# Performance work log

Measured on AMD Instinct MI355X. Metric: run time of the kernel, lower is better.

## Reference

```python
import jax, jax.numpy as jnp
import numpy as np

D_MODEL = 2048
NUM_TILES = 64
D_SLICE = D_MODEL // NUM_TILES  # 32
TILES_PER_CLUSTER = 8
NUM_CLUSTERS = NUM_TILES // TILES_PER_CLUSTER  # 8
GRID = 16
LN_EPS = 1e-5

# per-tile owned dimension indices: (tile_id*d_slice + j) % d_model  -> disjoint contiguous slices
DIMS = (np.arange(NUM_TILES)[:, None] * D_SLICE + np.arange(D_SLICE)[None, :]) % D_MODEL  # [T, d_slice]
DIMS = jnp.asarray(DIMS, dtype=jnp.int32)


def setup_inputs() -> dict:
    key = jax.random.key(0)
    k1, k2, k3, k4, k5, k6 = jax.random.split(key, 6)
    x = jax.random.normal(k1, (4, 4096, D_MODEL), dtype=jnp.float32)
    ln_gamma = 1.0 + 0.1 * jax.random.normal(k2, (D_MODEL,), dtype=jnp.float32)
    ln_beta = 0.1 * jax.random.normal(k3, (D_MODEL,), dtype=jnp.float32)
    spline_bases = 0.1 * jax.random.normal(k4, (NUM_TILES, D_SLICE, GRID), dtype=jnp.float32)
    spline_slopes = 0.1 + 0.1 * jax.random.normal(k5, (NUM_TILES, D_SLICE, GRID), dtype=jnp.float32)
    output_scale = 1.0 + 0.1 * jax.random.normal(k6, (NUM_TILES,), dtype=jnp.float32)
    return {"x": x, "ln_gamma": ln_gamma, "ln_beta": ln_beta,
            "spline_bases": spline_bases, "spline_slopes": spline_slopes,
            "output_scale": output_scale}


def _forward(x, ln_gamma, ln_beta, spline_bases, spline_slopes, output_scale):
    B, S, D = x.shape
    N = B * S
    # --- input LayerNorm (eval mode, dropout is identity) ---
    mu = jnp.mean(x, axis=-1, keepdims=True)
    var = jnp.mean(jnp.square(x - mu), axis=-1, keepdims=True)
    xn = (x - mu) * jax.lax.rsqrt(var + LN_EPS) * ln_gamma + ln_beta
    xf = xn.reshape(N, D)

    # --- tile / cluster signatures (hierarchy built from fresh EMA = current sigs) ---
    slope_sign = jnp.sign(jnp.mean(spline_slopes, axis=-1))           # [T, d_slice]
    tile_sigs = jnp.zeros((NUM_TILES, D), dtype=x.dtype)
    tile_sigs = tile_sigs.at[jnp.arange(NUM_TILES)[:, None], DIMS].set(slope_sign)  # [T, D]
    cluster_sigs = jnp.sign(tile_sigs.reshape(NUM_CLUSTERS, TILES_PER_CLUSTER, D).mean(axis=1))  # [C, D]
    cluster_assign = jnp.arange(NUM_TILES, dtype=jnp.int32) // TILES_PER_CLUSTER  # [T]

    # --- two-level routing ---
    input_sigs = jnp.sign(xf)                                          # [N, D]
    cluster_scores = input_sigs @ cluster_sigs.T                       # [N, C]
    best_cluster = jnp.argmax(cluster_scores, axis=-1)                 # [N]
    tile_scores = input_sigs @ tile_sigs.T                             # [N, T]
    in_cluster = cluster_assign[None, :] == best_cluster[:, None]      # [N, T]
    tile_idx = jnp.argmax(jnp.where(in_cluster, tile_scores, -jnp.inf), axis=-1)  # [N]

    # --- per-tile KAN spline evaluation on owned slice ---
    tok_dims = DIMS[tile_idx]                                          # [N, d_slice]
    x_slice = jnp.take_along_axis(xf, tok_dims, axis=1)                # [N, d_slice]
    # per-tile scalar min/max over all routed tokens and slice dims (matches x_slice.min()/.max())
    tok_min = x_slice.min(axis=1)                                      # [N]
    tok_max = x_slice.max(axis=1)
    onehot = tile_idx[None, :] == jnp.arange(NUM_TILES)[:, None]       # [T, N]
    tile_min = jnp.where(onehot, tok_min[None, :], jnp.inf).min(axis=1)    # [T]
    tile_max = jnp.where(onehot, tok_max[None, :], -jnp.inf).max(axis=1)   # [T]
    mn = tile_min[tile_idx][:, None]
    mx = tile_max[tile_idx][:, None]
    u = jnp.clip((x_slice - mn) / (mx - mn + 1e-8), 0.0, 1.0 - 1e-6)   # [N, d_slice]
    gi = jnp.clip((u * GRID).astype(jnp.int32), 0, GRID - 1)           # [N, d_slice]
    j = jnp.arange(D_SLICE)[None, :]
    b = spline_bases[tile_idx[:, None], j, gi]                         # [N, d_slice]
    s = spline_slopes[tile_idx[:, None], j, gi]
    x_local = (u - gi.astype(u.dtype) / GRID) * GRID
    delta = (b + s * x_local) * output_scale[tile_idx][:, None]        # [N, d_slice]

    # --- scatter delta into tile's slice (tile use_residual=False -> zeros elsewhere) ---
    out = jnp.zeros_like(xf).at[jnp.arange(N)[:, None], tok_dims].set(delta)
    # FFN residual bus
    return x + out.reshape(B, S, D)


def reference(x, ln_gamma, ln_beta, spline_bases, spline_slopes, output_scale):
    return _forward(x, ln_gamma, ln_beta, spline_bases, spline_slopes, output_scale)
```

## Files before the change

kernel.cpp:

```cpp
#include <hip/hip_runtime.h>

#define D_MODEL 2048
#define NUM_TILES 64
#define D_SLICE 32
#define TILES_PER_CLUSTER 8
#define NUM_CLUSTERS 8
#define GRID_PTS 16
#define LN_EPS 1e-5f
#define NBUCKET 64

typedef float f32x4 __attribute__((ext_vector_type(4)));

__device__ __forceinline__ unsigned int encF(float f) {
    unsigned int u = __float_as_uint(f);
    return (u & 0x80000000u) ? ~u : (u | 0x80000000u);
}
__device__ __forceinline__ float decF(unsigned int u) {
    unsigned int b = (u & 0x80000000u) ? (u ^ 0x80000000u) : ~u;
    return __uint_as_float(b);
}

__global__ void kan_setup(const float* __restrict__ slopes,
                          float* __restrict__ sgn,
                          unsigned int* __restrict__ tminb,
                          unsigned int* __restrict__ tmaxb) {
    int d = blockIdx.x * blockDim.x + threadIdx.x;
    if (d < NUM_TILES * NBUCKET) { tminb[d] = 0xFFFFFFFFu; tmaxb[d] = 0u; }
    if (d < D_MODEL) {
        const float* p = slopes + (size_t)d * GRID_PTS;
        float s = 0.f;
#pragma unroll
        for (int k = 0; k < GRID_PTS; ++k) s += p[k];
        float m = s * (1.0f / GRID_PTS);
        sgn[d] = (m > 0.f) ? 1.f : ((m < 0.f) ? -1.f : 0.f);
    }
}

__launch_bounds__(256)
__global__ void kan_main(const float* __restrict__ x,
                         const float* __restrict__ gamma,
                         const float* __restrict__ beta,
                         const float* __restrict__ sgn,
                         float* __restrict__ out,
                         float* __restrict__ xn_slice,
                         int* __restrict__ tidx_out,
                         unsigned int* __restrict__ tminb,
                         unsigned int* __restrict__ tmaxb) {
    const int wid = threadIdx.x >> 6;
    const int l   = threadIdx.x & 63;
    const int k   = l >> 3;
    const int n   = blockIdx.x * 4 + wid;
    const size_t rowb = (size_t)n * D_MODEL;

    const float* xr = x + rowb + 4 * l;
    f32x4 xc0 = *(const f32x4*)(xr);
    f32x4 xc1 = *(const f32x4*)(xr + 256);
    f32x4 xc2 = *(const f32x4*)(xr + 512);
    f32x4 xc3 = *(const f32x4*)(xr + 768);
    f32x4 xc4 = *(const f32x4*)(xr + 1024);
    f32x4 xc5 = *(const f32x4*)(xr + 1280);
    f32x4 xc6 = *(const f32x4*)(xr + 1536);
    f32x4 xc7 = *(const f32x4*)(xr + 1792);

    float* orow = out + rowb + 4 * l;
    *(f32x4*)(orow)        = xc0;
    *(f32x4*)(orow + 256)  = xc1;
    *(f32x4*)(orow + 512)  = xc2;
    *(f32x4*)(orow + 768)  = xc3;
    *(f32x4*)(orow + 1024) = xc4;
    *(f32x4*)(orow + 1280) = xc5;
    *(f32x4*)(orow + 1536) = xc6;
    *(f32x4*)(orow + 1792) = xc7;

    float s = 0.f, q = 0.f;
#define ACC(V) { s += V.x + V.y + V.z + V.w; \
                 q += V.x*V.x + V.y*V.y + V.z*V.z + V.w*V.w; }
    ACC(xc0) ACC(xc1) ACC(xc2) ACC(xc3) ACC(xc4) ACC(xc5) ACC(xc6) ACC(xc7)
#undef ACC
#pragma unroll
    for (int off = 32; off > 0; off >>= 1) {
        s += __shfl_xor(s, off);
        q += __shfl_xor(q, off);
    }
    const float mu = s * (1.0f / D_MODEL);
    float var = q * (1.0f / D_MODEL) - mu * mu;
    var = fmaxf(var, 0.0f);
    const float rs = rsqrtf(var + LN_EPS);

    const float* gp = gamma + 4 * l;
    const float* bp = beta + 4 * l;
    const float* sp = sgn + 4 * l;
    int cs0, cs1, cs2, cs3, cs4, cs5, cs6, cs7;
    int kw0, kw1, kw2, kw3, kw4, kw5, kw6, kw7;

#define CHUNK(c, XC, CS, KW)                                               \
    {                                                                      \
        f32x4 g  = *(const f32x4*)(gp + 256 * c);                          \
        f32x4 bb = *(const f32x4*)(bp + 256 * c);                          \
        f32x4 sg = *(const f32x4*)(sp + 256 * c);                          \
        float n0 = (XC.x - mu) * rs * g.x + bb.x;                          \
        float n1 = (XC.y - mu) * rs * g.y + bb.y;                          \
        float n2 = (XC.z - mu) * rs * g.z + bb.z;                          \
        float n3 = (XC.w - mu) * rs * g.w + bb.w;                          \
        int sc = ((n0 > 0.f) - (n0 < 0.f)) * (int)sg.x                     \
               + ((n1 > 0.f) - (n1 < 0.f)) * (int)sg.y                     \
               + ((n2 > 0.f) - (n2 < 0.f)) * (int)sg.z                     \
               + ((n3 > 0.f) - (n3 < 0.f)) * (int)sg.w;                    \
        sc += __shfl_xor(sc, 1);                                           \
        sc += __shfl_xor(sc, 2);                                           \
        sc += __shfl_xor(sc, 4);      \
        int cm = sc;                                                       \
        cm += __shfl_xor(cm, 8);                                           \
        cm += __shfl_xor(cm, 16);                                          \
        cm += __shfl_xor(cm, 32);           \
        CS = cm;                                                           \
        int key = ((sc + 64) << 3) | (7 - k);                              \
        key = max(key, __shfl_xor(key, 8));                                \
        key = max(key, __shfl_xor(key, 16));                               \
        key = max(key, __shfl_xor(key, 32));             \
        KW = 7 - (key & 7);       \
    }
    CHUNK(0, xc0, cs0, kw0)
    CHUNK(1, xc1, cs1, kw1)
    CHUNK(2, xc2, cs2, kw2)
    CHUNK(3, xc3, cs3, kw3)
    CHUNK(4, xc4, cs4, kw4)
    CHUNK(5, xc5, cs5, kw5)
    CHUNK(6, xc6, cs6, kw6)
    CHUNK(7, xc7, cs7, kw7)
#undef CHUNK

    int bc = 0, bv = cs0;
    if (cs1 > bv) { bv = cs1; bc = 1; }
    if (cs2 > bv) { bv = cs2; bc = 2; }
    if (cs3 > bv) { bv = cs3; bc = 3; }
    if (cs4 > bv) { bv = cs4; bc = 4; }
    if (cs5 > bv) { bv = cs5; bc = 5; }
    if (cs6 > bv) { bv = cs6; bc = 6; }
    if (cs7 > bv) { bv = cs7; bc = 7; }
    const int kwin = (bc == 0) ? kw0 : (bc == 1) ? kw1 : (bc == 2) ? kw2 :
                     (bc == 3) ? kw3 : (bc == 4) ? kw4 : (bc == 5) ? kw5 :
                     (bc == 6) ? kw6 : kw7;
    const int tile = bc * 8 + kwin;

    if (l == 0) tidx_out[n] = tile;

    if (k == kwin) {
        const int doff = 256 * bc + 4 * l;
        f32x4 xs = *(const f32x4*)(x + rowb + doff);
        f32x4 g  = *(const f32x4*)(gamma + doff);
        f32x4 bb = *(const f32x4*)(beta + doff);
        f32x4 xn4;
        xn4.x = (xs.x - mu) * rs * g.x + bb.x;
        xn4.y = (xs.y - mu) * rs * g.y + bb.y;
        xn4.z = (xs.z - mu) * rs * g.z + bb.z;
        xn4.w = (xs.w - mu) * rs * g.w + bb.w;

        *(f32x4*)(xn_slice + (size_t)n * D_SLICE + 4 * (l & 7)) = xn4;

        float mn = fminf(fminf(xn4.x, xn4.y), fminf(xn4.z, xn4.w));
        float mx = fmaxf(fmaxf(xn4.x, xn4.y), fmaxf(xn4.z, xn4.w));
        mn = fminf(mn, __shfl_xor(mn, 1));
        mn = fminf(mn, __shfl_xor(mn, 2));
        mn = fminf(mn, __shfl_xor(mn, 4));
        mx = fmaxf(mx, __shfl_xor(mx, 1));
        mx = fmaxf(mx, __shfl_xor(mx, 2));
        mx = fmaxf(mx, __shfl_xor(mx, 4));
        if ((l & 7) == 0) {
            int bkt = n & (NBUCKET - 1);
            atomicMin(&tminb[tile * NBUCKET + bkt], encF(mn));
            atomicMax(&tmaxb[tile * NBUCKET + bkt], encF(mx));
        }
    }
}

__global__ void kan_reduce(const unsigned int* __restrict__ tminb,
                           const unsigned int* __restrict__ tmaxb,
                           unsigned int* __restrict__ tmin,
                           unsigned int* __restrict__ tmax) {
    int t = threadIdx.x;
    unsigned int mn = 0xFFFFFFFFu, mx = 0u;
#pragma unroll 4
    for (int b = 0; b < NBUCKET; ++b) {
        mn = min(mn, tminb[t * NBUCKET + b]);
        mx = max(mx, tmaxb[t * NBUCKET + b]);
    }
    tmin[t] = mn;
    tmax[t] = mx;
}

__global__ void kan_apply(const float* __restrict__ xn_slice,
                          const int* __restrict__ tidx,
                          const float* __restrict__ bases,
                          const float* __restrict__ slopes,
                          const float* __restrict__ oscale,
                          const unsigned int* __restrict__ tmin,
                          const unsigned int* __restrict__ tmax,
                          float* __restrict__ out, int N) {
    int g = blockIdx.x * blockDim.x + threadIdx.x;
    if (g >= N * 8) return;
    int n = g >> 3;
    int qd = g & 7;
    int t = tidx[n];
    f32x4 xn4 = *(const f32x4*)(xn_slice + (size_t)n * D_SLICE + qd * 4);
    float mn = decF(tmin[t]);
    float mx = decF(tmax[t]);
    float inv = 1.0f / (mx - mn + 1e-8f);
    float osc = oscale[t];

    float dl[4];
    float xnv[4] = {xn4.x, xn4.y, xn4.z, xn4.w};
#pragma unroll
    for (int e = 0; e < 4; ++e) {
        float u = (xnv[e] - mn) * inv;
        u = fminf(fmaxf(u, 0.0f), 1.0f - 1e-6f);
        int gi = (int)(u * (float)GRID_PTS);
        gi = min(max(gi, 0), GRID_PTS - 1);
        int j = qd * 4 + e;
        int off = (t * D_SLICE + j) * GRID_PTS + gi;
        float xl = (u - (float)gi * (1.0f / GRID_PTS)) * (float)GRID_PTS;
        dl[e] = (bases[off] + slopes[off] * xl) * osc;
    }
    size_t oi = (size_t)n * D_MODEL + t * D_SLICE + qd * 4;
    f32x4 o = *(f32x4*)(out + oi);
    o.x += dl[0]; o.y += dl[1]; o.z += dl[2]; o.w += dl[3];
    *(f32x4*)(out + oi) = o;
}

extern "C" void kernel_launch(void* const* d_in, const int* in_sizes, int n_in,
                              void* d_out, int out_size, void* d_ws, size_t ws_size,
                              hipStream_t stream) {
    const float* x      = (const float*)d_in[0];
    const float* gamma  = (const float*)d_in[1];
    const float* beta   = (const float*)d_in[2];
    const float* bases  = (const float*)d_in[3];
    const float* slopes = (const float*)d_in[4];
    const float* oscale = (const float*)d_in[5];
    float* out = (float*)d_out;
    const int N = in_sizes[0] / D_MODEL;

    char* w = (char*)d_ws;
    unsigned int* tminb = (unsigned int*)w; w += NUM_TILES * NBUCKET * 4;
    unsigned int* tmaxb = (unsigned int*)w; w += NUM_TILES * NBUCKET * 4;
    unsigned int* tmin  = (unsigned int*)w; w += 256;
    unsigned int* tmax  = (unsigned int*)w; w += 256;
    float* sgn = (float*)w;  w += D_MODEL * sizeof(float);
    int* tidx = (int*)w;     w += (size_t)N * sizeof(int);
    float* xns = (float*)w;  w += (size_t)N * D_SLICE * sizeof(float);

    kan_setup<<<(NUM_TILES * NBUCKET + 255) / 256, 256, 0, stream>>>(slopes, sgn, tminb, tmaxb);
    kan_main<<<N / 4, 256, 0, stream>>>(x, gamma, beta, sgn, out, xns, tidx, tminb, tmaxb);
    kan_reduce<<<1, 64, 0, stream>>>(tminb, tmaxb, tmin, tmax);
    kan_apply<<<(N * 8 + 255) / 256, 256, 0, stream>>>(xns, tidx, bases, slopes,
                                                       oscale, tmin, tmax, out, N);
}
```

Measured before the change: 65.20 us.

## Process four tokens per wavefront with double-buffered row prefetch

The main LayerNorm/routing kernel now has each wavefront handle four consecutive tokens instead of one. It keeps two register buffers, loading the next token's row while processing the current one, and the grid shrinks fourfold. The goal is to hide global load latency in this memory-bound kernel through software pipelining. In exchange it doubles the registers used for row data, which may lower occupancy, and it cuts the number of blocks in flight.

```diff
diff --git a/kernel.cpp b/kernel.cpp
--- a/kernel.cpp
+++ b/kernel.cpp
@@ -36,31 +36,21 @@
     }
 }
 
-__launch_bounds__(256)
-__global__ void kan_main(const float* __restrict__ x,
-                         const float* __restrict__ gamma,
-                         const float* __restrict__ beta,
-                         const float* __restrict__ sgn,
-                         float* __restrict__ out,
-                         float* __restrict__ xn_slice,
-                         int* __restrict__ tidx_out,
-                         unsigned int* __restrict__ tminb,
-                         unsigned int* __restrict__ tmaxb) {
-    const int wid = threadIdx.x >> 6;
-    const int l   = threadIdx.x & 63;
-    const int k   = l >> 3;
-    const int n   = blockIdx.x * 4 + wid;
+__device__ __forceinline__ void process_token(
+    f32x4 xc0, f32x4 xc1, f32x4 xc2, f32x4 xc3,
+    f32x4 xc4, f32x4 xc5, f32x4 xc6, f32x4 xc7,
+    int n, int l, int k,
+    const float* __restrict__ x,
+    const float* __restrict__ gamma,
+    const float* __restrict__ beta,
+    const float* __restrict__ sgn,
+    float* __restrict__ out,
+    float* __restrict__ xn_slice,
+    int* __restrict__ tidx_out,
+    unsigned int* __restrict__ tminb,
+    unsigned int* __restrict__ tmaxb)
+{
     const size_t rowb = (size_t)n * D_MODEL;
-
-    const float* xr = x + rowb + 4 * l;
-    f32x4 xc0 = *(const f32x4*)(xr);
-    f32x4 xc1 = *(const f32x4*)(xr + 256);
-    f32x4 xc2 = *(const f32x4*)(xr + 512);
-    f32x4 xc3 = *(const f32x4*)(xr + 768);
-    f32x4 xc4 = *(const f32x4*)(xr + 1024);
-    f32x4 xc5 = *(const f32x4*)(xr + 1280);
-    f32x4 xc6 = *(const f32x4*)(xr + 1536);
-    f32x4 xc7 = *(const f32x4*)(xr + 1792);
 
     float* orow = out + rowb + 4 * l;
     *(f32x4*)(orow)        = xc0;
@@ -174,6 +164,46 @@
     }
 }
 
+__launch_bounds__(256)
+__global__ void kan_main(const float* __restrict__ x,
+                         const float* __restrict__ gamma,
+                         const float* __restrict__ beta,
+                         const float* __restrict__ sgn,
+                         float* __restrict__ out,
+                         float* __restrict__ xn_slice,
+                         int* __restrict__ tidx_out,
+                         unsigned int* __restrict__ tminb,
+                         unsigned int* __restrict__ tmaxb) {
+    const int wid = threadIdx.x >> 6;
+    const int l   = threadIdx.x & 63;
+    const int k   = l >> 3;
+    const int gw  = blockIdx.x * 4 + wid;
+    const int n0  = gw * 4;
+
+#define LOADX(P, nn) { const float* xr_ = x + (size_t)(nn) * D_MODEL + 4 * l; \
+    P##0 = *(const f32x4*)(xr_);        P##1 = *(const f32x4*)(xr_ + 256);    \
+    P##2 = *(const f32x4*)(xr_ + 512);  P##3 = *(const f32x4*)(xr_ + 768);    \
+    P##4 = *(const f32x4*)(xr_ + 1024); P##5 = *(const f32x4*)(xr_ + 1280);   \
+    P##6 = *(const f32x4*)(xr_ + 1536); P##7 = *(const f32x4*)(xr_ + 1792); }
+
+    f32x4 a0, a1, a2, a3, a4, a5, a6, a7;
+    f32x4 b0, b1, b2, b3, b4, b5, b6, b7;
+
+    LOADX(a, n0)
+    LOADX(b, n0 + 1)
+    process_token(a0, a1, a2, a3, a4, a5, a6, a7, n0, l, k,
+                  x, gamma, beta, sgn, out, xn_slice, tidx_out, tminb, tmaxb);
+    LOADX(a, n0 + 2)
+    process_token(b0, b1, b2, b3, b4, b5, b6, b7, n0 + 1, l, k,
+                  x, gamma, beta, sgn, out, xn_slice, tidx_out, tminb, tmaxb);
+    LOADX(b, n0 + 3)
+    process_token(a0, a1, a2, a3, a4, a5, a6, a7, n0 + 2, l, k,
+                  x, gamma, beta, sgn, out, xn_slice, tidx_out, tminb, tmaxb);
+    process_token(b0, b1, b2, b3, b4, b5, b6, b7, n0 + 3, l, k,
+                  x, gamma, beta, sgn, out, xn_slice, tidx_out, tminb, tmaxb);
+#undef LOADX
+}
+
 __global__ void kan_reduce(const unsigned int* __restrict__ tminb,
                            const unsigned int* __restrict__ tmaxb,
                            unsigned int* __restrict__ tmin,
@@ -249,7 +279,7 @@
     float* xns = (float*)w;  w += (size_t)N * D_SLICE * sizeof(float);
 
     kan_setup<<<(NUM_TILES * NBUCKET + 255) / 256, 256, 0, stream>>>(slopes, sgn, tminb, tmaxb);
-    kan_main<<<N / 4, 256, 0, stream>>>(x, gamma, beta, sgn, out, xns, tidx, tminb, tmaxb);
+    kan_main<<<N / 16, 256, 0, stream>>>(x, gamma, beta, sgn, out, xns, tidx, tminb, tmaxb);
     kan_reduce<<<1, 64, 0, stream>>>(tminb, tmaxb, tmin, tmax);
     kan_apply<<<(N * 8 + 255) / 256, 256, 0, stream>>>(xns, tidx, bases, slopes,
                                                        oscale, tmin, tmax, out, N);
```

Result: slower. 74.98 us (+15.0%).
